# Optimization experiments

Measured on AMD Instinct MI355X. Metric: run time of the kernel, lower is better.

## Reference

```python
import jax, jax.numpy as jnp
import numpy as np

SCALE = 0.125  # (dim // heads) ** -0.5 = (256 // 4) ** -0.5


def setup_inputs() -> dict:
    key = jax.random.key(0)
    k1, k2, k3, k4, k5 = jax.random.split(key, 5)
    dim, red = 256, 4
    c = dim // red  # 64
    B, H, W = 4, 64, 64
    x = jax.random.normal(k1, (B, dim, H, W), dtype=jnp.float32)
    qkv_w = jax.random.normal(k2, (3 * c, dim), dtype=jnp.float32) * 0.02
    qkv_b = jax.random.normal(k3, (3 * c,), dtype=jnp.float32) * 0.02
    proj_w = jax.random.normal(k4, (dim, c), dtype=jnp.float32) * 0.02
    proj_b = jax.random.normal(k5, (dim,), dtype=jnp.float32) * 0.02
    return {"x": x, "qkv_w": qkv_w, "qkv_b": qkv_b, "proj_w": proj_w, "proj_b": proj_b}


def reference(x, qkv_w, qkv_b, proj_w, proj_b):
    B, C, H, W = x.shape
    # 1x1 conv == channel matmul
    qkv = jnp.einsum('bchw,oc->bohw', x, qkv_w) + qkv_b[None, :, None, None]
    c = qkv.shape[1] // 3
    qkv = qkv.reshape(B, 3 * c, H * W)
    q, k, v = qkv[:, :c], qkv[:, c:2 * c], qkv[:, 2 * c:]  # [B, c, HW]
    # attn[b, n, m] = sum_c q[b,c,n] * k[b,c,m] * scale
    attn = jnp.einsum('bcn,bcm->bnm', q, k) * SCALE
    attn = jax.nn.softmax(attn, axis=-1)  # [B, HW, HW]
    # out[b, c, n] = sum_m v[b,c,m] * attn[b,n,m]   (v @ attn^T)
    out = jnp.einsum('bcm,bnm->bcn', v, attn).reshape(B, c, H, W)
    # proj 1x1 conv back to dim
    return jnp.einsum('bchw,oc->bohw', out, proj_w) + proj_b[None, :, None, None]
```

## Files before the change

### kernel.cpp

```cpp
#include <hip/hip_runtime.h>
#include <hip/hip_bf16.h>


#define N_TOK 4096
#define CDIM  64
#define DIM   256
#define NBAT  4

typedef __attribute__((ext_vector_type(8)))  short          short8;
typedef __attribute__((ext_vector_type(8)))  unsigned short ushort8_t;
typedef __attribute__((ext_vector_type(4)))  unsigned short ushort4_t;
typedef __attribute__((ext_vector_type(4)))  unsigned int   uint4_t;
typedef __attribute__((ext_vector_type(4)))  float          float4_t;
typedef __attribute__((ext_vector_type(16))) float          float16_t;

#if __has_builtin(__builtin_amdgcn_exp2f)
#define QSC  0.18033688011112042f
#define PEXP(x) __builtin_amdgcn_exp2f(x)
#else
#define QSC  0.125f
#define PEXP(x) __expf(x)
#endif

__device__ __forceinline__ unsigned short f2bf(float f) {
  unsigned int u = __builtin_bit_cast(unsigned int, f);
  u += 0x7fffu + ((u >> 16) & 1u);
  return (unsigned short)(u >> 16);
}

__device__ __forceinline__ unsigned int pkcv(float a, float b) {
  __hip_bfloat162 h = __float22bfloat162_rn(make_float2(a, b));
  unsigned int r; __builtin_memcpy(&r, &h, 4); return r;
}

__device__ __forceinline__ short8 ld8(const unsigned short* p) {
  return __builtin_bit_cast(short8, *(const ushort8_t*)p);
}

__device__ __forceinline__ short8 pack8f(float4_t a, float4_t b) {
  uint4_t u;
  u[0] = pkcv(a[0], a[1]); u[1] = pkcv(a[2], a[3]);
  u[2] = pkcv(b[0], b[1]); u[3] = pkcv(b[2], b[3]);
  return __builtin_bit_cast(short8, u);
}

__device__ __forceinline__ float16_t z16() {
  float16_t r;
#pragma unroll
  for (int i = 0; i < 16; ++i) r[i] = 0.0f;
  return r;
}

typedef __attribute__((address_space(1))) const void* gvp;
typedef __attribute__((address_space(3))) void*       lvp;
__device__ __forceinline__ void dma16(const unsigned short* g, unsigned short* l) {
  __builtin_amdgcn_global_load_lds((gvp)g, (lvp)l, 16, 0, 0);
}

#define MFMA(a, b, c) __builtin_amdgcn_mfma_f32_32x32x16_bf16((a), (b), (c), 0, 0, 0)

#define QOFF  0
#define KOFF  1048576
#define VOFF  2097152
#define WQOFF 3145728
#define BSOFF 3194880

__global__ void k_prep(const float* __restrict__ qw, const float* __restrict__ qb,
                       unsigned short* __restrict__ wqs, float* __restrict__ bs)
{
  const int g = blockIdx.x * 256 + threadIdx.x;
  {
    const int lane = g & 63, grp = g >> 6;
    const int w6 = grp >> 4, kk = grp & 15;
    const int o = w6 * 32 + (lane & 31);
    const int c = kk * 16 + (lane >> 5) * 8;
    const float sc = (o < 64) ? QSC : 1.0f;
    const float* src = qw + o * 256 + c;
    ushort8_t u;
#pragma unroll
    for (int j = 0; j < 8; ++j) u[j] = f2bf(src[j] * sc);
    *(ushort8_t*)(wqs + g * 8) = u;
  }
  if (g < 48) {
    float4_t f = *(const float4_t*)(qb + g * 4);
    float4_t o;
#pragma unroll
    for (int j = 0; j < 4; ++j) o[j] = f[j] * ((g * 4 + j) < 64 ? QSC : 1.0f);
    *(float4_t*)(bs + g * 4) = o;
  }
}

#define RS 132

__global__ __launch_bounds__(384, 2) void k_qkv(
    const float* __restrict__ x, const unsigned short* __restrict__ wqs,
    const float* __restrict__ bs, unsigned short* __restrict__ Qf,
    unsigned short* __restrict__ Kf, unsigned short* __restrict__ Vf)
{
  __shared__ unsigned int Xl[64 * RS];
  const int id = blockIdx.x;
  const int b  = (id >> 1) & 3;
  const int nt = (id & 1) | ((id >> 3) << 1);
  const int t  = threadIdx.x;
  const int n0g = nt * 64;

  if (t < 256) {
    const int n0  = (t & 15) * 4;
    const int cpb = t >> 4;
#pragma unroll
    for (int p = 0; p < 8; ++p) {
      const int cp = cpb + 16 * p, c = cp * 2;
      const float* xb = x + (((size_t)(b * DIM + c)) << 12) + n0g + n0;
      float4_t a = *(const float4_t*)xb;
      float4_t d = *(const float4_t*)(xb + 4096);
#pragma unroll
      for (int j = 0; j < 4; ++j)
        Xl[(n0 + j) * RS + cp] = pkcv(a[j], d[j]);
    }
  }
  __syncthreads();

  const int w = t >> 6, lane = t & 63, l31 = lane & 31, lh = lane >> 5;
  const unsigned short* wrow = wqs + ((w * 16) << 9) + lane * 8;
  const unsigned int*   xr0  = &Xl[l31 * RS + lh * 4];
  const unsigned int*   xr1  = &Xl[(32 + l31) * RS + lh * 4];

  float16_t a0 = z16(), a1 = z16();
  if (w < 4) {
#pragma unroll
    for (int kk = 0; kk < 16; ++kk) {
      short8 wf = ld8(wrow + (kk << 9));
      short8 x0 = __builtin_bit_cast(short8, *(const uint4_t*)(xr0 + kk * 8));
      short8 x1 = __builtin_bit_cast(short8, *(const uint4_t*)(xr1 + kk * 8));
      a0 = MFMA(wf, x0, a0);
      a1 = MFMA(wf, x1, a1);
    }
  } else {
#pragma unroll
    for (int kk = 0; kk < 16; ++kk) {
      short8 wf = ld8(wrow + (kk << 9));
      short8 x0 = __builtin_bit_cast(short8, *(const uint4_t*)(xr0 + kk * 8));
      short8 x1 = __builtin_bit_cast(short8, *(const uint4_t*)(xr1 + kk * 8));
      a0 = MFMA(x0, wf, a0);
      a1 = MFMA(x1, wf, a1);
    }
  }

  if (w < 4) {
    unsigned short* dst = (w < 2) ? Qf : Kf;
    const int w2 = w & 1;
#pragma unroll
    for (int sub = 0; sub < 2; ++sub) {
      const float16_t& aa = sub ? a1 : a0;
      const int ch = nt * 2 + sub;
#pragma unroll
      for (int p = 0; p < 4; ++p) {
        const int o = w * 32 + p * 8 + lh * 4;
        float4_t bv = *(const float4_t*)(bs + o);
        ushort4_t pk4;
#pragma unroll
        for (int q = 0; q < 4; ++q) pk4[q] = f2bf(aa[p * 4 + q] + bv[q]);
        const int kkt = w2 * 2 + (p >> 1);
        *(ushort4_t*)(dst + ((((b * 128 + ch) * 4 + kkt) << 9)
                             + (l31 + 32 * (p & 1)) * 8 + lh * 4)) = pk4;
      }
    }
  } else {
    const int ct = w - 4;
    const float bvs = bs[128 + ct * 32 + l31];
#pragma unroll
    for (int sub = 0; sub < 2; ++sub) {
      const float16_t& aa = sub ? a1 : a0;
      const int ch = nt * 2 + sub;
#pragma unroll
      for (int ks = 0; ks < 2; ++ks) {
        ushort8_t pk8;
#pragma unroll
        for (int j = 0; j < 8; ++j) pk8[j] = f2bf(aa[ks * 8 + j] + bvs);
        *(ushort8_t*)(Vf + ((((b * 128 + ch) * 4 + ct * 2 + ks) << 9)
                            + lane * 8)) = pk8;
      }
    }
  }
}

#define OS   68
#define OLS  72
#define NACC (64 * OS + 64)

__global__ __launch_bounds__(512, 1) void k_attn(
    const unsigned short* __restrict__ Qf, const unsigned short* __restrict__ Kf,
    const unsigned short* __restrict__ Vf, const float* __restrict__ pw,
    const float* __restrict__ pb, float* __restrict__ out)
{
  __shared__ __align__(16) unsigned short KV[2][2][16384];
  __shared__ float Oacc[NACC];
  __shared__ __align__(16) unsigned short Ol[64 * OLS];

  const int id = blockIdx.x;
  const int b  = (id >> 1) & 3;
  const int nt = (id & 1) | ((id >> 3) << 1);
  const int t  = threadIdx.x;
  const int wv = t >> 6, lane = t & 63, l31 = lane & 31, lh = lane >> 5;
  const int mq = wv >> 1, nsub = wv & 1;

  for (int i = t; i < NACC; i += 512) Oacc[i] = 0.0f;

  const int kvsel = wv >> 2;
  const int wq2   = (wv & 3) * 2;
  const unsigned short* sg = ((kvsel == 0) ? Kf : Vf)
                             + (((size_t)(b * 128 + wq2)) << 11) + lane * 8;

  short8 qf[4];
#pragma unroll
  for (int kk = 0; kk < 4; ++kk)
    qf[kk] = ld8(Qf + (((b * 128 + nt * 2 + nsub) * 4 + kk) << 9) + lane * 8);

#pragma unroll
  for (int c2 = 0; c2 < 2; ++c2)
#pragma unroll
    for (int kk = 0; kk < 4; ++kk)
      dma16(sg + (c2 << 11) + (kk << 9),
            &KV[0][kvsel][((wq2 + c2) << 11) + (kk << 9)]);

  float16_t oc0 = z16(), oc1 = z16();
  float den = 0.0f;

  __syncthreads();

  for (int t4 = 0; t4 < 16; ++t4) {
    const int cur = t4 & 1;

    if (t4 < 15) {
      const unsigned short* g = sg + (((size_t)(t4 + 1)) << 14);
#pragma unroll
      for (int c2 = 0; c2 < 2; ++c2)
#pragma unroll
        for (int kk = 0; kk < 4; ++kk)
          dma16(g + (c2 << 11) + (kk << 9),
                &KV[cur ^ 1][kvsel][((wq2 + c2) << 11) + (kk << 9)]);
    }

#pragma unroll
    for (int cc = 0; cc < 2; ++cc) {
      const int ch = mq * 2 + cc;
      const unsigned short* kl = &KV[cur][0][ch << 11];
      const unsigned short* vl = &KV[cur][1][ch << 11];

      short8 kf0 = ld8(kl + lane * 8);
      short8 kf1 = ld8(kl + 512 + lane * 8);
      short8 kf2 = ld8(kl + 1024 + lane * 8);
      short8 kf3 = ld8(kl + 1536 + lane * 8);

      float16_t s = z16();
      s = MFMA(kf0, qf[0], s);
      s = MFMA(kf1, qf[1], s);
      s = MFMA(kf2, qf[2], s);
      s = MFMA(kf3, qf[3], s);

      float p[16];
#pragma unroll
      for (int e = 0; e < 16; ++e) p[e] = PEXP(s[e]);
      {
        float d0 = (p[0] + p[1]) + (p[2] + p[3]);
        float d1 = (p[4] + p[5]) + (p[6] + p[7]);
        float d2 = (p[8] + p[9]) + (p[10] + p[11]);
        float d3 = (p[12] + p[13]) + (p[14] + p[15]);
        den += (d0 + d1) + (d2 + d3);
      }

      uint4_t w0, w1;
#pragma unroll
      for (int j = 0; j < 4; ++j) {
        w0[j] = pkcv(p[2 * j], p[2 * j + 1]);
        w1[j] = pkcv(p[8 + 2 * j], p[9 + 2 * j]);
      }
      short8 pf0 = __builtin_bit_cast(short8, w0);
      short8 pf1 = __builtin_bit_cast(short8, w1);

      short8 vf0 = ld8(vl + lane * 8);
      short8 vf1 = ld8(vl + 512 + lane * 8);
      short8 vf2 = ld8(vl + 1024 + lane * 8);
      short8 vf3 = ld8(vl + 1536 + lane * 8);

      oc0 = MFMA(pf0, vf0, oc0);
      oc0 = MFMA(pf1, vf1, oc0);
      oc1 = MFMA(pf0, vf2, oc1);
      oc1 = MFMA(pf1, vf3, oc1);
    }

    __syncthreads();
  }

  den += __shfl_xor(den, 32);

#pragma unroll
  for (int ct = 0; ct < 2; ++ct) {
    const float16_t& oa = ct ? oc1 : oc0;
    const int cc = ct * 32 + l31;
#pragma unroll
    for (int e = 0; e < 16; ++e) {
      const int nr = nsub * 32 + (e & 3) + 8 * (e >> 2) + 4 * lh;
      atomicAdd(&Oacc[nr * OS + cc], oa[e]);
    }
  }
  if (lane < 32) atomicAdd(&Oacc[64 * OS + nsub * 32 + l31], den);
  __syncthreads();

  {
    const int nloc = t >> 3, c8 = (t & 7) * 8;
    float4_t s0 = *(float4_t*)&Oacc[nloc * OS + c8];
    float4_t s1 = *(float4_t*)&Oacc[nloc * OS + c8 + 4];
    const float r = 1.0f / Oacc[64 * OS + nloc];
    uint4_t o4;
    o4[0] = pkcv(s0[0] * r, s0[1] * r);
    o4[1] = pkcv(s0[2] * r, s0[3] * r);
    o4[2] = pkcv(s1[0] * r, s1[1] * r);
    o4[3] = pkcv(s1[2] * r, s1[3] * r);
    *(uint4_t*)&Ol[nloc * OLS + c8] = o4;
  }
  __syncthreads();

  float16_t f0 = z16(), f1 = z16();
  const float* pwrow = pw + (wv * 32 + l31) * 64 + lh * 8;
#pragma unroll
  for (int kk = 0; kk < 4; ++kk) {
    float4_t wa = *(const float4_t*)(pwrow + kk * 16);
    float4_t wb = *(const float4_t*)(pwrow + kk * 16 + 4);
    short8 af = pack8f(wa, wb);
    short8 b0 = ld8(&Ol[l31 * OLS + kk * 16 + lh * 8]);
    short8 b1 = ld8(&Ol[(32 + l31) * OLS + kk * 16 + lh * 8]);
    f0 = MFMA(af, b0, f0);
    f1 = MFMA(af, b1, f1);
  }
  const int n0 = nt * 64;
#pragma unroll
  for (int e = 0; e < 16; ++e) {
    const int o = wv * 32 + (e & 3) + 8 * (e >> 2) + 4 * lh;
    const float bv = pb[o];
    out[((b * 256 + o) << 12) + n0 + l31]      = f0[e] + bv;
    out[((b * 256 + o) << 12) + n0 + 32 + l31] = f1[e] + bv;
  }
}

extern "C" void kernel_launch(void* const* d_in, const int* in_sizes, int n_in,
                              void* d_out, int out_size, void* d_ws, size_t ws_size,
                              hipStream_t stream) {
  const float* x      = (const float*)d_in[0];
  const float* qkv_w  = (const float*)d_in[1];
  const float* qkv_b  = (const float*)d_in[2];
  const float* proj_w = (const float*)d_in[3];
  const float* proj_b = (const float*)d_in[4];
  float* out = (float*)d_out;

  unsigned short* ws  = (unsigned short*)d_ws;
  unsigned short* qf  = ws + QOFF;
  unsigned short* kf  = ws + KOFF;
  unsigned short* vf  = ws + VOFF;
  unsigned short* wqs = ws + WQOFF;
  float*          bs  = (float*)(ws + BSOFF);

  k_prep<<<24, 256, 0, stream>>>(qkv_w, qkv_b, wqs, bs);
  k_qkv<<<256, 384, 0, stream>>>(x, wqs, bs, qf, kf, vf);
  k_attn<<<256, 512, 0, stream>>>(qf, kf, vf, proj_w, proj_b, out);
}
```

Before: 132.2 us.

## Fuse prep, QKV projection and attention into one cooperative kernel

Merges the weight-prep, QKV projection and attention kernels into a single cooperative kernel with a grid-wide sync between the projection and attention phases. Weights are converted to bf16 in registers, so the separate prep pass and its workspace round-trip go away. Shared memory is aliased between the x tile and the K/V buffers. The softmax denominator is now computed with an extra MFMA against a ones vector instead of VALU adds, and the two extra kernel launches are removed. The grid-wide barrier costs something in its own right and requires all 256 blocks to be co-resident, and launch bounds now ask for 2 blocks per CU despite the large shared-memory footprint.

```diff
diff --git a/kernel.cpp b/kernel.cpp
--- a/kernel.cpp
+++ b/kernel.cpp
@@ -1,5 +1,6 @@
 #include <hip/hip_runtime.h>
 #include <hip/hip_bf16.h>
+#include <hip/hip_cooperative_groups.h>
 
 
 #define N_TOK 4096
@@ -10,23 +11,13 @@
 typedef __attribute__((ext_vector_type(8)))  short          short8;
 typedef __attribute__((ext_vector_type(8)))  unsigned short ushort8_t;
 typedef __attribute__((ext_vector_type(4)))  unsigned short ushort4_t;
+typedef __attribute__((ext_vector_type(2)))  unsigned int   uint2_t;
 typedef __attribute__((ext_vector_type(4)))  unsigned int   uint4_t;
 typedef __attribute__((ext_vector_type(4)))  float          float4_t;
 typedef __attribute__((ext_vector_type(16))) float          float16_t;
 
-#if __has_builtin(__builtin_amdgcn_exp2f)
 #define QSC  0.18033688011112042f
 #define PEXP(x) __builtin_amdgcn_exp2f(x)
-#else
-#define QSC  0.125f
-#define PEXP(x) __expf(x)
-#endif
-
-__device__ __forceinline__ unsigned short f2bf(float f) {
-  unsigned int u = __builtin_bit_cast(unsigned int, f);
-  u += 0x7fffu + ((u >> 16) & 1u);
-  return (unsigned short)(u >> 16);
-}
 
 __device__ __forceinline__ unsigned int pkcv(float a, float b) {
   __hip_bfloat162 h = __float22bfloat162_rn(make_float2(a, b));
@@ -62,146 +53,131 @@
 #define QOFF  0
 #define KOFF  1048576
 #define VOFF  2097152
-#define WQOFF 3145728
-#define BSOFF 3194880
-
-__global__ void k_prep(const float* __restrict__ qw, const float* __restrict__ qb,
-                       unsigned short* __restrict__ wqs, float* __restrict__ bs)
-{
-  const int g = blockIdx.x * 256 + threadIdx.x;
-  {
-    const int lane = g & 63, grp = g >> 6;
-    const int w6 = grp >> 4, kk = grp & 15;
-    const int o = w6 * 32 + (lane & 31);
-    const int c = kk * 16 + (lane >> 5) * 8;
-    const float sc = (o < 64) ? QSC : 1.0f;
-    const float* src = qw + o * 256 + c;
-    ushort8_t u;
-#pragma unroll
-    for (int j = 0; j < 8; ++j) u[j] = f2bf(src[j] * sc);
-    *(ushort8_t*)(wqs + g * 8) = u;
-  }
-  if (g < 48) {
-    float4_t f = *(const float4_t*)(qb + g * 4);
-    float4_t o;
-#pragma unroll
-    for (int j = 0; j < 4; ++j) o[j] = f[j] * ((g * 4 + j) < 64 ? QSC : 1.0f);
-    *(float4_t*)(bs + g * 4) = o;
-  }
-}
-
-#define RS 132
-
-__global__ __launch_bounds__(384, 2) void k_qkv(
-    const float* __restrict__ x, const unsigned short* __restrict__ wqs,
-    const float* __restrict__ bs, unsigned short* __restrict__ Qf,
-    unsigned short* __restrict__ Kf, unsigned short* __restrict__ Vf)
-{
-  __shared__ unsigned int Xl[64 * RS];
-  const int id = blockIdx.x;
-  const int b  = (id >> 1) & 3;
-  const int nt = (id & 1) | ((id >> 3) << 1);
-  const int t  = threadIdx.x;
-  const int n0g = nt * 64;
-
-  if (t < 256) {
-    const int n0  = (t & 15) * 4;
-    const int cpb = t >> 4;
-#pragma unroll
-    for (int p = 0; p < 8; ++p) {
-      const int cp = cpb + 16 * p, c = cp * 2;
-      const float* xb = x + (((size_t)(b * DIM + c)) << 12) + n0g + n0;
-      float4_t a = *(const float4_t*)xb;
-      float4_t d = *(const float4_t*)(xb + 4096);
-#pragma unroll
-      for (int j = 0; j < 4; ++j)
-        Xl[(n0 + j) * RS + cp] = pkcv(a[j], d[j]);
-    }
-  }
-  __syncthreads();
-
-  const int w = t >> 6, lane = t & 63, l31 = lane & 31, lh = lane >> 5;
-  const unsigned short* wrow = wqs + ((w * 16) << 9) + lane * 8;
-  const unsigned int*   xr0  = &Xl[l31 * RS + lh * 4];
-  const unsigned int*   xr1  = &Xl[(32 + l31) * RS + lh * 4];
-
-  float16_t a0 = z16(), a1 = z16();
-  if (w < 4) {
-#pragma unroll
-    for (int kk = 0; kk < 16; ++kk) {
-      short8 wf = ld8(wrow + (kk << 9));
-      short8 x0 = __builtin_bit_cast(short8, *(const uint4_t*)(xr0 + kk * 8));
-      short8 x1 = __builtin_bit_cast(short8, *(const uint4_t*)(xr1 + kk * 8));
-      a0 = MFMA(wf, x0, a0);
-      a1 = MFMA(wf, x1, a1);
-    }
-  } else {
-#pragma unroll
-    for (int kk = 0; kk < 16; ++kk) {
-      short8 wf = ld8(wrow + (kk << 9));
-      short8 x0 = __builtin_bit_cast(short8, *(const uint4_t*)(xr0 + kk * 8));
-      short8 x1 = __builtin_bit_cast(short8, *(const uint4_t*)(xr1 + kk * 8));
-      a0 = MFMA(x0, wf, a0);
-      a1 = MFMA(x1, wf, a1);
-    }
-  }
-
-  if (w < 4) {
-    unsigned short* dst = (w < 2) ? Qf : Kf;
-    const int w2 = w & 1;
-#pragma unroll
-    for (int sub = 0; sub < 2; ++sub) {
-      const float16_t& aa = sub ? a1 : a0;
-      const int ch = nt * 2 + sub;
-#pragma unroll
-      for (int p = 0; p < 4; ++p) {
-        const int o = w * 32 + p * 8 + lh * 4;
-        float4_t bv = *(const float4_t*)(bs + o);
-        ushort4_t pk4;
-#pragma unroll
-        for (int q = 0; q < 4; ++q) pk4[q] = f2bf(aa[p * 4 + q] + bv[q]);
-        const int kkt = w2 * 2 + (p >> 1);
-        *(ushort4_t*)(dst + ((((b * 128 + ch) * 4 + kkt) << 9)
-                             + (l31 + 32 * (p & 1)) * 8 + lh * 4)) = pk4;
-      }
-    }
-  } else {
-    const int ct = w - 4;
-    const float bvs = bs[128 + ct * 32 + l31];
-#pragma unroll
-    for (int sub = 0; sub < 2; ++sub) {
-      const float16_t& aa = sub ? a1 : a0;
-      const int ch = nt * 2 + sub;
-#pragma unroll
-      for (int ks = 0; ks < 2; ++ks) {
-        ushort8_t pk8;
-#pragma unroll
-        for (int j = 0; j < 8; ++j) pk8[j] = f2bf(aa[ks * 8 + j] + bvs);
-        *(ushort8_t*)(Vf + ((((b * 128 + ch) * 4 + ct * 2 + ks) << 9)
-                            + lane * 8)) = pk8;
-      }
-    }
-  }
-}
-
+
+#define RS   132
 #define OS   68
 #define OLS  72
 #define NACC (64 * OS + 64)
 
-__global__ __launch_bounds__(512, 1) void k_attn(
-    const unsigned short* __restrict__ Qf, const unsigned short* __restrict__ Kf,
-    const unsigned short* __restrict__ Vf, const float* __restrict__ pw,
-    const float* __restrict__ pb, float* __restrict__ out)
+#define SM_BYTES (131072 + NACC * 4 + 64 * OLS * 2)
+
+__global__ __launch_bounds__(512, 2) void k_fused(
+    const float* __restrict__ x, const float* __restrict__ qw,
+    const float* __restrict__ qb, unsigned short* __restrict__ Qf,
+    unsigned short* __restrict__ Kf, unsigned short* __restrict__ Vf,
+    const float* __restrict__ pw, const float* __restrict__ pb,
+    float* __restrict__ out)
 {
-  __shared__ __align__(16) unsigned short KV[2][2][16384];
-  __shared__ float Oacc[NACC];
-  __shared__ __align__(16) unsigned short Ol[64 * OLS];
+  __shared__ __align__(16) unsigned char SM[SM_BYTES];
+  unsigned short* KVb = (unsigned short*)SM;
+  float*          Oacc = (float*)(SM + 131072);
+  unsigned short* Ol   = (unsigned short*)(SM + 131072 + NACC * 4);
+  unsigned int*   Xl   = (unsigned int*)SM;
 
   const int id = blockIdx.x;
   const int b  = (id >> 1) & 3;
   const int nt = (id & 1) | ((id >> 3) << 1);
   const int t  = threadIdx.x;
   const int wv = t >> 6, lane = t & 63, l31 = lane & 31, lh = lane >> 5;
+
+  {
+    const int n0g = nt * 64;
+
+    short8 wf[16];
+    if (wv < 6) {
+      const float sc = (wv < 2) ? QSC : 1.0f;
+      const float* wbase = qw + (wv * 32 + l31) * 256 + lh * 8;
+#pragma unroll
+      for (int kk = 0; kk < 16; ++kk) {
+        float4_t a = *(const float4_t*)(wbase + kk * 16);
+        float4_t c = *(const float4_t*)(wbase + kk * 16 + 4);
+#pragma unroll
+        for (int j = 0; j < 4; ++j) { a[j] *= sc; c[j] *= sc; }
+        wf[kk] = pack8f(a, c);
+      }
+    }
+
+    {
+      const int n0  = (t & 15) * 4;
+      const int cpb = t >> 4;
+#pragma unroll
+      for (int p = 0; p < 4; ++p) {
+        const int cp = cpb + 32 * p, c = cp * 2;
+        const float* xb = x + (((size_t)(b * DIM + c)) << 12) + n0g + n0;
+        float4_t a = *(const float4_t*)xb;
+        float4_t d = *(const float4_t*)(xb + 4096);
+#pragma unroll
+        for (int j = 0; j < 4; ++j)
+          Xl[(n0 + j) * RS + cp] = pkcv(a[j], d[j]);
+      }
+    }
+    __syncthreads();
+
+    if (wv < 6) {
+      const unsigned int* xr0 = &Xl[l31 * RS + lh * 4];
+      const unsigned int* xr1 = &Xl[(32 + l31) * RS + lh * 4];
+      float16_t a0 = z16(), a1 = z16();
+      if (wv < 4) {
+#pragma unroll
+        for (int kk = 0; kk < 16; ++kk) {
+          short8 x0 = __builtin_bit_cast(short8, *(const uint4_t*)(xr0 + kk * 8));
+          short8 x1 = __builtin_bit_cast(short8, *(const uint4_t*)(xr1 + kk * 8));
+          a0 = MFMA(wf[kk], x0, a0);
+          a1 = MFMA(wf[kk], x1, a1);
+        }
+      } else {
+#pragma unroll
+        for (int kk = 0; kk < 16; ++kk) {
+          short8 x0 = __builtin_bit_cast(short8, *(const uint4_t*)(xr0 + kk * 8));
+          short8 x1 = __builtin_bit_cast(short8, *(const uint4_t*)(xr1 + kk * 8));
+          a0 = MFMA(x0, wf[kk], a0);
+          a1 = MFMA(x1, wf[kk], a1);
+        }
+      }
+
+      if (wv < 4) {
+        unsigned short* dst = (wv < 2) ? Qf : Kf;
+        const int w2 = wv & 1;
+        const float bsc = (wv < 2) ? QSC : 1.0f;
+#pragma unroll
+        for (int sub = 0; sub < 2; ++sub) {
+          const float16_t& aa = sub ? a1 : a0;
+          const int ch = nt * 2 + sub;
+#pragma unroll
+          for (int p = 0; p < 4; ++p) {
+            const int o = wv * 32 + p * 8 + lh * 4;
+            float4_t bv = *(const float4_t*)(qb + o);
+            uint2_t u2;
+            u2[0] = pkcv(aa[p * 4 + 0] + bv[0] * bsc, aa[p * 4 + 1] + bv[1] * bsc);
+            u2[1] = pkcv(aa[p * 4 + 2] + bv[2] * bsc, aa[p * 4 + 3] + bv[3] * bsc);
+            const int kkt = w2 * 2 + (p >> 1);
+            *(uint2_t*)(dst + ((((b * 128 + ch) * 4 + kkt) << 9)
+                               + (l31 + 32 * (p & 1)) * 8 + lh * 4)) = u2;
+          }
+        }
+      } else {
+        const int ct = wv - 4;
+        const float bvs = qb[128 + ct * 32 + l31];
+#pragma unroll
+        for (int sub = 0; sub < 2; ++sub) {
+          const float16_t& aa = sub ? a1 : a0;
+          const int ch = nt * 2 + sub;
+#pragma unroll
+          for (int ks = 0; ks < 2; ++ks) {
+            uint4_t u4;
+#pragma unroll
+            for (int j = 0; j < 4; ++j)
+              u4[j] = pkcv(aa[ks * 8 + 2 * j] + bvs, aa[ks * 8 + 2 * j + 1] + bvs);
+            *(uint4_t*)(Vf + ((((b * 128 + ch) * 4 + ct * 2 + ks) << 9)
+                              + lane * 8)) = u4;
+          }
+        }
+      }
+    }
+  }
+
+  cooperative_groups::this_grid().sync();
+
   const int mq = wv >> 1, nsub = wv & 1;
 
   for (int i = t; i < NACC; i += 512) Oacc[i] = 0.0f;
@@ -210,21 +186,25 @@
   const int wq2   = (wv & 3) * 2;
   const unsigned short* sg = ((kvsel == 0) ? Kf : Vf)
                              + (((size_t)(b * 128 + wq2)) << 11) + lane * 8;
+  unsigned short* KVbase = KVb + kvsel * 16384;
 
   short8 qf[4];
 #pragma unroll
   for (int kk = 0; kk < 4; ++kk)
     qf[kk] = ld8(Qf + (((b * 128 + nt * 2 + nsub) * 4 + kk) << 9) + lane * 8);
 
+  uint4_t one4; one4[0] = 0x3F803F80u; one4[1] = 0x3F803F80u;
+  one4[2] = 0x3F803F80u; one4[3] = 0x3F803F80u;
+  const short8 ONES = __builtin_bit_cast(short8, one4);
+
 #pragma unroll
   for (int c2 = 0; c2 < 2; ++c2)
 #pragma unroll
     for (int kk = 0; kk < 4; ++kk)
       dma16(sg + (c2 << 11) + (kk << 9),
-            &KV[0][kvsel][((wq2 + c2) << 11) + (kk << 9)]);
-
-  float16_t oc0 = z16(), oc1 = z16();
-  float den = 0.0f;
+            KVbase + ((wq2 + c2) << 11) + (kk << 9));
+
+  float16_t oc0 = z16(), oc1 = z16(), dacc = z16();
 
   __syncthreads();
 
@@ -233,19 +213,20 @@
 
     if (t4 < 15) {
       const unsigned short* g = sg + (((size_t)(t4 + 1)) << 14);
+      unsigned short* ldst = KVbase + (cur ^ 1) * 32768;
 #pragma unroll
       for (int c2 = 0; c2 < 2; ++c2)
 #pragma unroll
         for (int kk = 0; kk < 4; ++kk)
           dma16(g + (c2 << 11) + (kk << 9),
-                &KV[cur ^ 1][kvsel][((wq2 + c2) << 11) + (kk << 9)]);
+                ldst + ((wq2 + c2) << 11) + (kk << 9));
     }
 
 #pragma unroll
     for (int cc = 0; cc < 2; ++cc) {
       const int ch = mq * 2 + cc;
-      const unsigned short* kl = &KV[cur][0][ch << 11];
-      const unsigned short* vl = &KV[cur][1][ch << 11];
+      const unsigned short* kl = KVb + cur * 32768 + (ch << 11);
+      const unsigned short* vl = KVb + cur * 32768 + 16384 + (ch << 11);
 
       short8 kf0 = ld8(kl + lane * 8);
       short8 kf1 = ld8(kl + 512 + lane * 8);
@@ -261,13 +242,6 @@
       float p[16];
 #pragma unroll
       for (int e = 0; e < 16; ++e) p[e] = PEXP(s[e]);
-      {
-        float d0 = (p[0] + p[1]) + (p[2] + p[3]);
-        float d1 = (p[4] + p[5]) + (p[6] + p[7]);
-        float d2 = (p[8] + p[9]) + (p[10] + p[11]);
-        float d3 = (p[12] + p[13]) + (p[14] + p[15]);
-        den += (d0 + d1) + (d2 + d3);
-      }
 
       uint4_t w0, w1;
 #pragma unroll
@@ -283,16 +257,16 @@
       short8 vf2 = ld8(vl + 1024 + lane * 8);
       short8 vf3 = ld8(vl + 1536 + lane * 8);
 
-      oc0 = MFMA(pf0, vf0, oc0);
-      oc0 = MFMA(pf1, vf1, oc0);
-      oc1 = MFMA(pf0, vf2, oc1);
-      oc1 = MFMA(pf1, vf3, oc1);
+      oc0  = MFMA(pf0, vf0, oc0);
+      oc0  = MFMA(pf1, vf1, oc0);
+      oc1  = MFMA(pf0, vf2, oc1);
+      oc1  = MFMA(pf1, vf3, oc1);
+      dacc = MFMA(pf0, ONES, dacc);
+      dacc = MFMA(pf1, ONES, dacc);
     }
 
     __syncthreads();
   }
-
-  den += __shfl_xor(den, 32);
 
 #pragma unroll
   for (int ct = 0; ct < 2; ++ct) {
@@ -304,7 +278,13 @@
       atomicAdd(&Oacc[nr * OS + cc], oa[e]);
     }
   }
-  if (lane < 32) atomicAdd(&Oacc[64 * OS + nsub * 32 + l31], den);
+  if (l31 == 0) {
+#pragma unroll
+    for (int e = 0; e < 16; ++e) {
+      const int nr = nsub * 32 + (e & 3) + 8 * (e >> 2) + 4 * lh;
+      atomicAdd(&Oacc[64 * OS + nr], dacc[e]);
+    }
+  }
   __syncthreads();
 
   {
@@ -351,16 +331,16 @@
   const float* qkv_b  = (const float*)d_in[2];
   const float* proj_w = (const float*)d_in[3];
   const float* proj_b = (const float*)d_in[4];
-  float* out = (float*)d_out;
-
-  unsigned short* ws  = (unsigned short*)d_ws;
-  unsigned short* qf  = ws + QOFF;
-  unsigned short* kf  = ws + KOFF;
-  unsigned short* vf  = ws + VOFF;
-  unsigned short* wqs = ws + WQOFF;
-  float*          bs  = (float*)(ws + BSOFF);
-
-  k_prep<<<24, 256, 0, stream>>>(qkv_w, qkv_b, wqs, bs);
-  k_qkv<<<256, 384, 0, stream>>>(x, wqs, bs, qf, kf, vf);
-  k_attn<<<256, 512, 0, stream>>>(qf, kf, vf, proj_w, proj_b, out);
-}
+  float* outp = (float*)d_out;
+
+  unsigned short* ws = (unsigned short*)d_ws;
+  unsigned short* qf = ws + QOFF;
+  unsigned short* kf = ws + KOFF;
+  unsigned short* vf = ws + VOFF;
+
+  void* args[] = { (void*)&x, (void*)&qkv_w, (void*)&qkv_b,
+                   (void*)&qf, (void*)&kf, (void*)&vf,
+                   (void*)&proj_w, (void*)&proj_b, (void*)&outp };
+  hipLaunchCooperativeKernel((const void*)k_fused, dim3(256), dim3(512),
+                             args, 0, stream);
+}
```

Result: slower. 174.0 us (+31.7%).

## Swizzle QKV LDS layout, remap block ids, compute softmax denominator via MFMA

Applied to the files above, without the earlier changes.

Replaces the padded LDS row stride for the staged x tile with an XOR swizzle to avoid bank conflicts without padding. Changes the block-to-(batch, token tile) mapping in both kernels and packs bf16 outputs with the paired conversion intrinsic. The softmax denominator is now accumulated with extra MFMAs against a ones vector instead of scalar adds and a shuffle, trading two matrix ops per step for fewer VALU adds. The denominator is summed from the bf16-rounded probabilities, so it now matches exactly what multiplies V.

```diff
diff --git a/kernel.cpp b/kernel.cpp
--- a/kernel.cpp
+++ b/kernel.cpp
@@ -10,17 +10,13 @@
 typedef __attribute__((ext_vector_type(8)))  short          short8;
 typedef __attribute__((ext_vector_type(8)))  unsigned short ushort8_t;
 typedef __attribute__((ext_vector_type(4)))  unsigned short ushort4_t;
+typedef __attribute__((ext_vector_type(2)))  unsigned int   uint2_t;
 typedef __attribute__((ext_vector_type(4)))  unsigned int   uint4_t;
 typedef __attribute__((ext_vector_type(4)))  float          float4_t;
 typedef __attribute__((ext_vector_type(16))) float          float16_t;
 
-#if __has_builtin(__builtin_amdgcn_exp2f)
 #define QSC  0.18033688011112042f
 #define PEXP(x) __builtin_amdgcn_exp2f(x)
-#else
-#define QSC  0.125f
-#define PEXP(x) __expf(x)
-#endif
 
 __device__ __forceinline__ unsigned short f2bf(float f) {
   unsigned int u = __builtin_bit_cast(unsigned int, f);
@@ -90,17 +86,19 @@
   }
 }
 
-#define RS 132
+__device__ __forceinline__ int xsw(int n, int cp) {
+  return n * 128 + ((((cp >> 2) ^ ((n >> 2) & 7)) << 2) | (cp & 3));
+}
 
 __global__ __launch_bounds__(384, 2) void k_qkv(
     const float* __restrict__ x, const unsigned short* __restrict__ wqs,
     const float* __restrict__ bs, unsigned short* __restrict__ Qf,
     unsigned short* __restrict__ Kf, unsigned short* __restrict__ Vf)
 {
-  __shared__ unsigned int Xl[64 * RS];
+  __shared__ unsigned int Xl[64 * 128];
   const int id = blockIdx.x;
-  const int b  = (id >> 1) & 3;
-  const int nt = (id & 1) | ((id >> 3) << 1);
+  const int b  = id & 3;
+  const int nt = id >> 2;
   const int t  = threadIdx.x;
   const int n0g = nt * 64;
 
@@ -115,32 +113,34 @@
       float4_t d = *(const float4_t*)(xb + 4096);
 #pragma unroll
       for (int j = 0; j < 4; ++j)
-        Xl[(n0 + j) * RS + cp] = pkcv(a[j], d[j]);
+        Xl[xsw(n0 + j, cp)] = pkcv(a[j], d[j]);
     }
   }
   __syncthreads();
 
   const int w = t >> 6, lane = t & 63, l31 = lane & 31, lh = lane >> 5;
   const unsigned short* wrow = wqs + ((w * 16) << 9) + lane * 8;
-  const unsigned int*   xr0  = &Xl[l31 * RS + lh * 4];
-  const unsigned int*   xr1  = &Xl[(32 + l31) * RS + lh * 4];
+  const unsigned int*   xb0  = &Xl[l31 * 128];
+  const int sw = (l31 >> 2) & 7;
 
   float16_t a0 = z16(), a1 = z16();
   if (w < 4) {
 #pragma unroll
     for (int kk = 0; kk < 16; ++kk) {
+      const int idx = ((lh + 2 * kk) ^ sw) << 2;
       short8 wf = ld8(wrow + (kk << 9));
-      short8 x0 = __builtin_bit_cast(short8, *(const uint4_t*)(xr0 + kk * 8));
-      short8 x1 = __builtin_bit_cast(short8, *(const uint4_t*)(xr1 + kk * 8));
+      short8 x0 = __builtin_bit_cast(short8, *(const uint4_t*)(xb0 + idx));
+      short8 x1 = __builtin_bit_cast(short8, *(const uint4_t*)(xb0 + 4096 + idx));
       a0 = MFMA(wf, x0, a0);
       a1 = MFMA(wf, x1, a1);
     }
   } else {
 #pragma unroll
     for (int kk = 0; kk < 16; ++kk) {
+      const int idx = ((lh + 2 * kk) ^ sw) << 2;
       short8 wf = ld8(wrow + (kk << 9));
-      short8 x0 = __builtin_bit_cast(short8, *(const uint4_t*)(xr0 + kk * 8));
-      short8 x1 = __builtin_bit_cast(short8, *(const uint4_t*)(xr1 + kk * 8));
+      short8 x0 = __builtin_bit_cast(short8, *(const uint4_t*)(xb0 + idx));
+      short8 x1 = __builtin_bit_cast(short8, *(const uint4_t*)(xb0 + 4096 + idx));
       a0 = MFMA(x0, wf, a0);
       a1 = MFMA(x1, wf, a1);
     }
@@ -157,12 +157,12 @@
       for (int p = 0; p < 4; ++p) {
         const int o = w * 32 + p * 8 + lh * 4;
         float4_t bv = *(const float4_t*)(bs + o);
-        ushort4_t pk4;
-#pragma unroll
-        for (int q = 0; q < 4; ++q) pk4[q] = f2bf(aa[p * 4 + q] + bv[q]);
+        uint2_t u2;
+        u2[0] = pkcv(aa[p * 4 + 0] + bv[0], aa[p * 4 + 1] + bv[1]);
+        u2[1] = pkcv(aa[p * 4 + 2] + bv[2], aa[p * 4 + 3] + bv[3]);
         const int kkt = w2 * 2 + (p >> 1);
-        *(ushort4_t*)(dst + ((((b * 128 + ch) * 4 + kkt) << 9)
-                             + (l31 + 32 * (p & 1)) * 8 + lh * 4)) = pk4;
+        *(uint2_t*)(dst + ((((b * 128 + ch) * 4 + kkt) << 9)
+                           + (l31 + 32 * (p & 1)) * 8 + lh * 4)) = u2;
       }
     }
   } else {
@@ -174,11 +174,12 @@
       const int ch = nt * 2 + sub;
 #pragma unroll
       for (int ks = 0; ks < 2; ++ks) {
-        ushort8_t pk8;
-#pragma unroll
-        for (int j = 0; j < 8; ++j) pk8[j] = f2bf(aa[ks * 8 + j] + bvs);
-        *(ushort8_t*)(Vf + ((((b * 128 + ch) * 4 + ct * 2 + ks) << 9)
-                            + lane * 8)) = pk8;
+        uint4_t u4;
+#pragma unroll
+        for (int j = 0; j < 4; ++j)
+          u4[j] = pkcv(aa[ks * 8 + 2 * j] + bvs, aa[ks * 8 + 2 * j + 1] + bvs);
+        *(uint4_t*)(Vf + ((((b * 128 + ch) * 4 + ct * 2 + ks) << 9)
+                          + lane * 8)) = u4;
       }
     }
   }
@@ -198,8 +199,8 @@
   __shared__ __align__(16) unsigned short Ol[64 * OLS];
 
   const int id = blockIdx.x;
-  const int b  = (id >> 1) & 3;
-  const int nt = (id & 1) | ((id >> 3) << 1);
+  const int b  = id & 3;
+  const int nt = id >> 2;
   const int t  = threadIdx.x;
   const int wv = t >> 6, lane = t & 63, l31 = lane & 31, lh = lane >> 5;
   const int mq = wv >> 1, nsub = wv & 1;
@@ -216,6 +217,10 @@
   for (int kk = 0; kk < 4; ++kk)
     qf[kk] = ld8(Qf + (((b * 128 + nt * 2 + nsub) * 4 + kk) << 9) + lane * 8);
 
+  uint4_t one4; one4[0] = 0x3F803F80u; one4[1] = 0x3F803F80u;
+  one4[2] = 0x3F803F80u; one4[3] = 0x3F803F80u;
+  const short8 ONES = __builtin_bit_cast(short8, one4);
+
 #pragma unroll
   for (int c2 = 0; c2 < 2; ++c2)
 #pragma unroll
@@ -223,8 +228,7 @@
       dma16(sg + (c2 << 11) + (kk << 9),
             &KV[0][kvsel][((wq2 + c2) << 11) + (kk << 9)]);
 
-  float16_t oc0 = z16(), oc1 = z16();
-  float den = 0.0f;
+  float16_t oc0 = z16(), oc1 = z16(), dacc = z16();
 
   __syncthreads();
 
@@ -261,13 +265,6 @@
       float p[16];
 #pragma unroll
       for (int e = 0; e < 16; ++e) p[e] = PEXP(s[e]);
-      {
-        float d0 = (p[0] + p[1]) + (p[2] + p[3]);
-        float d1 = (p[4] + p[5]) + (p[6] + p[7]);
-        float d2 = (p[8] + p[9]) + (p[10] + p[11]);
-        float d3 = (p[12] + p[13]) + (p[14] + p[15]);
-        den += (d0 + d1) + (d2 + d3);
-      }
 
       uint4_t w0, w1;
 #pragma unroll
@@ -283,16 +280,16 @@
       short8 vf2 = ld8(vl + 1024 + lane * 8);
       short8 vf3 = ld8(vl + 1536 + lane * 8);
 
-      oc0 = MFMA(pf0, vf0, oc0);
-      oc0 = MFMA(pf1, vf1, oc0);
-      oc1 = MFMA(pf0, vf2, oc1);
-      oc1 = MFMA(pf1, vf3, oc1);
+      oc0  = MFMA(pf0, vf0, oc0);
+      oc0  = MFMA(pf1, vf1, oc0);
+      oc1  = MFMA(pf0, vf2, oc1);
+      oc1  = MFMA(pf1, vf3, oc1);
+      dacc = MFMA(pf0, ONES, dacc);
+      dacc = MFMA(pf1, ONES, dacc);
     }
 
     __syncthreads();
   }
-
-  den += __shfl_xor(den, 32);
 
 #pragma unroll
   for (int ct = 0; ct < 2; ++ct) {
@@ -304,7 +301,13 @@
       atomicAdd(&Oacc[nr * OS + cc], oa[e]);
     }
   }
-  if (lane < 32) atomicAdd(&Oacc[64 * OS + nsub * 32 + l31], den);
+  if (l31 == 0) {
+#pragma unroll
+    for (int e = 0; e < 16; ++e) {
+      const int nr = nsub * 32 + (e & 3) + 8 * (e >> 2) + 4 * lh;
+      atomicAdd(&Oacc[64 * OS + nr], dacc[e]);
+    }
+  }
   __syncthreads();
 
   {
```

New measurement: 132.8 us. Within noise of the previous version (+0.5%).
